# Optimization experiments

Measured on AMD Instinct MI355X. Metric: run time of the kernel, lower is better.

The kernel has to match this reference:

```python
import jax, jax.numpy as jnp
import numpy as np

N, B, S, A = 4, 32768, 512, 64
H = 256          # hidden_size
NH = 16          # effective number of heads = attend_dim (range(attend_dim) bug in source)
D = 16           # attend_dim = hidden // attend_heads
EPS_BN = 1e-5


def setup_inputs() -> dict:
    key = jax.random.key(0)
    ks = jax.random.split(key, 16)
    sc = 0.05
    return {
        "states": jax.random.normal(ks[0], (N, B, S), dtype=jnp.float32),
        "actions": jax.random.normal(ks[1], (N, B, A), dtype=jnp.float32),
        # per-agent state+action encoder (enc_fc1)
        "Wenc": jax.random.normal(ks[2], (N, S + A, H), dtype=jnp.float32) * sc,
        "benc": jax.random.normal(ks[3], (N, H), dtype=jnp.float32) * sc,
        # per-agent state encoder (s_enc_fc1)
        "Ws": jax.random.normal(ks[4], (N, S, H), dtype=jnp.float32) * sc,
        "bs": jax.random.normal(ks[5], (N, H), dtype=jnp.float32) * sc,
        # shared per-head extractors (no bias on key/selector; bias on value)
        "Wk": jax.random.normal(ks[6], (NH, H, D), dtype=jnp.float32) * sc,
        "Wsel": jax.random.normal(ks[7], (NH, H, D), dtype=jnp.float32) * sc,
        "Wv": jax.random.normal(ks[8], (NH, H, D), dtype=jnp.float32) * sc,
        "bv": jax.random.normal(ks[9], (NH, D), dtype=jnp.float32) * sc,
        # per-agent critic MLP (input = H + NH*D = 2H)
        "Wc1": jax.random.normal(ks[10], (N, 2 * H, H), dtype=jnp.float32) * sc,
        "bc1": jax.random.normal(ks[11], (N, H), dtype=jnp.float32) * sc,
        "Wc2": jax.random.normal(ks[12], (N, H, A), dtype=jnp.float32) * sc,
        "bc2": jax.random.normal(ks[13], (N, A), dtype=jnp.float32) * sc,
    }


def _lrelu(x):
    return jax.nn.leaky_relu(x, 0.01)


def _bn(x):
    # BatchNorm1d(affine=False), training mode: biased batch stats over batch axis
    m = x.mean(axis=1, keepdims=True)
    v = x.var(axis=1, keepdims=True)
    return (x - m) * jax.lax.rsqrt(v + EPS_BN)


def reference(states, actions, Wenc, benc, Ws, bs, Wk, Wsel, Wv, bv, Wc1, bc1, Wc2, bc2):
    n, b = states.shape[0], states.shape[1]
    # state+action encodings per agent: [n, B, H]
    sa = jnp.concatenate([states, actions], axis=-1)
    sa_enc = _lrelu(jnp.einsum('nbi,nih->nbh', _bn(sa), Wenc) + benc[:, None, :])
    # state encodings per agent: [n, B, H]
    s_enc = _lrelu(jnp.einsum('nbs,nsh->nbh', _bn(states), Ws) + bs[:, None, :])
    # per-head keys/values/selectors: [NH, n, B, D]
    keys = jnp.einsum('nbh,ehd->enbd', sa_enc, Wk)
    vals = _lrelu(jnp.einsum('nbh,ehd->enbd', sa_enc, Wv) + bv[:, None, None, :])
    sel = jnp.einsum('nbh,ehd->enbd', s_enc, Wsel)
    # attention of agent i over agents j != i (self excluded via -inf mask)
    logits = jnp.einsum('eibd,ejbd->eibj', sel, keys) / jnp.sqrt(jnp.float32(D))
    self_mask = jnp.eye(n, dtype=bool)[None, :, None, :]  # [1, i, 1, j]
    probs = jax.nn.softmax(jnp.where(self_mask, -1e9, logits), axis=-1)
    # weighted values: [n, B, NH, D] (head-major concat order)
    other = jnp.einsum('eibj,ejbd->ibed', probs, vals)
    critic_in = jnp.concatenate([s_enc, other.reshape(n, b, NH * D)], axis=-1)  # [n, B, 2H]
    h = _lrelu(jnp.einsum('nbc,nch->nbh', critic_in, Wc1) + bc1[:, None, :])
    all_q = jnp.einsum('nbh,nha->nba', h, Wc2) + bc2[:, None, :]  # [n, B, A]
    idx = jnp.argmax(actions, axis=-1)  # [n, B]
    q = jnp.take_along_axis(all_q, idx[..., None], axis=-1)  # [n, B, 1]
    return q
```

## Files before the change

kernel.cpp:

```cpp
#include <hip/hip_runtime.h>
#include <hip/hip_bf16.h>
#include <cstdint>
#include <cstddef>

using bf16 = __hip_bfloat16;
typedef __attribute__((ext_vector_type(8))) short bf16x8v;
typedef __attribute__((ext_vector_type(4))) short bf16x4v;
typedef __attribute__((ext_vector_type(4))) float f32x4v;

constexpr int Nn = 4;
constexpr int Bb = 32768;
constexpr int Ss = 512;
constexpr int Av = 64;
constexpr int SA = 576;
constexpr float BN_EPS = 1e-5f;

__device__ __forceinline__ float lrelu(float v){ return v >= 0.f ? v : 0.01f * v; }
__device__ __forceinline__ float bf2f(bf16 x){ return __bfloat162float(x); }
__device__ __forceinline__ short f2bf(float v){
  union { bf16 b; short s; } u; u.b = __float2bfloat16(v); return u.s;
}

template<bool WRX>
__global__ __launch_bounds__(256) void conv_stats(const float* __restrict__ states,
                                                  const float* __restrict__ actions,
                                                  float* __restrict__ ssum,
                                                  float* __restrict__ ssq,
                                                  short* __restrict__ Xbf){
  const int n  = blockIdx.z;
  const int tx = threadIdx.x;
  const int ty = threadIdx.y;
  const int g  = blockIdx.x * 64 + tx;
  const bool on = g < (SA / 4);
  const int f  = g * 4;
  const float* p = nullptr; int step = 0;
  if (on){
    if (f < Ss){ p = states  + (size_t)n*Bb*Ss + f;        step = Ss; }
    else       { p = actions + (size_t)n*Bb*Av + (f - Ss); step = Av; }
  }
  float s0=0.f,s1=0.f,s2=0.f,s3=0.f,q0=0.f,q1=0.f,q2=0.f,q3=0.f;
  const int b0 = blockIdx.y * 512 + ty, bend = blockIdx.y * 512 + 512;
  if (on){
    for (int b = b0; b < bend; b += 4){
      float4 v = *(const float4*)(p + (size_t)b*step);
      if (WRX){
        short t4[4] __attribute__((aligned(8))) =
            { f2bf(v.x), f2bf(v.y), f2bf(v.z), f2bf(v.w) };
        *(bf16x4v*)&Xbf[((size_t)n*Bb + b)*SA + f] = *(bf16x4v*)t4;
      }
      s0 += v.x; q0 += v.x*v.x;
      s1 += v.y; q1 += v.y*v.y;
      s2 += v.z; q2 += v.z*v.z;
      s3 += v.w; q3 += v.w*v.w;
    }
  }
  __shared__ float rs[4][64][4], rq[4][64][4];
  rs[ty][tx][0]=s0; rs[ty][tx][1]=s1; rs[ty][tx][2]=s2; rs[ty][tx][3]=s3;
  rq[ty][tx][0]=q0; rq[ty][tx][1]=q1; rq[ty][tx][2]=q2; rq[ty][tx][3]=q3;
  __syncthreads();
  if (ty == 0 && on){
    #pragma unroll
    for (int j = 0; j < 4; j++){
      float ts = rs[0][tx][j]+rs[1][tx][j]+rs[2][tx][j]+rs[3][tx][j];
      float tq = rq[0][tx][j]+rq[1][tx][j]+rq[2][tx][j]+rq[3][tx][j];
      atomicAdd(&ssum[n*SA + f + j], ts);
      atomicAdd(&ssq [n*SA + f + j], tq);
    }
  }
}

__global__ void bn_finalize(const float* __restrict__ ssum, const float* __restrict__ ssq,
                            float* __restrict__ mean, float* __restrict__ rstd){
  int i = blockIdx.x * 256 + threadIdx.x;
  float m = ssum[i] * (1.f / Bb);
  float v = ssq[i] * (1.f / Bb) - m * m;
  v = fmaxf(v, 0.f);
  mean[i] = m;
  rstd[i] = rsqrtf(v + BN_EPS);
}

__global__ void bias_copy(const float* __restrict__ b1, const float* __restrict__ b2,
                          float* __restrict__ o1, float* __restrict__ o2){
  int i = blockIdx.x * 256 + threadIdx.x;
  if (i < Nn*256){ o1[i] = b1[i]; o2[i] = b2[i]; }
}

template<int HEAD>
__global__ __launch_bounds__(256) void foldT2(const float* __restrict__ src,
                                              const float* __restrict__ scale,
                                              const float* __restrict__ mean,
                                              float* __restrict__ bias_out,
                                              short* __restrict__ dst,
                                              int K, int N){
  const int a  = blockIdx.z;
  const int tx = threadIdx.x & 63;
  const int ty = threadIdx.x >> 6;
  const int f0 = blockIdx.x * 64 + ty * 16;
  const int c  = blockIdx.y * 64 + tx;
  const float* s = src + (HEAD ? 0 : (size_t)a*K*N);
  short tmp[16] __attribute__((aligned(16)));
  float bsum = 0.f;
  #pragma unroll
  for (int j = 0; j < 16; j++){
    const int f = f0 + j;
    float w = HEAD ? s[(((size_t)(c >> 4))*K + f)*16 + (c & 15)]
                   : s[(size_t)f*N + c];
    if (scale) w *= scale[a*SA + f];
    if (mean)  bsum += mean[a*SA + f] * w;
    tmp[j] = f2bf(w);
  }
  short* d = dst + (HEAD ? 0 : (size_t)a*K*N) + (size_t)c*K + f0;
  *(bf16x8v*)d       = *(bf16x8v*)tmp;
  *(bf16x8v*)(d + 8) = *(bf16x8v*)(tmp + 8);
  if (mean){
    __shared__ float red[4][64];
    red[ty][tx] = bsum;
    __syncthreads();
    if (threadIdx.x < 64){
      float t = red[0][threadIdx.x] + red[1][threadIdx.x]
              + red[2][threadIdx.x] + red[3][threadIdx.x];
      atomicAdd(&bias_out[a*N + blockIdx.y*64 + threadIdx.x], -t);
    }
  }
}

template<int BM,int BN,int WM,int WN,int K,int ASRC,int AP,bool ACT,bool OUTF32>
__global__ __launch_bounds__(256) void mgemm(const void* A1, const void* A2,
                                             const short* __restrict__ Wp, int wPerAgent,
                                             const float* __restrict__ bias, int biasStride,
                                             void* Out, int outPitch){
  __shared__ __align__(16) short As[BM*40];
  __shared__ __align__(16) short Bs[BN*40];
  const int tid  = threadIdx.x;
  const int a    = blockIdx.z;
  const int row0 = blockIdx.x * BM;
  const int col0 = blockIdx.y * BN;
  const short* Wb = Wp + (size_t)a * wPerAgent;
  constexpr int FM = BM/WM/16, FN = BN/WN/16;
  const int wid = tid >> 6, lane = tid & 63;
  const int wm = wid % WM, wn = wid / WM;
  const int rowB = wm*(BM/WM), colB = wn*(BN/WN);
  const int lrow = lane & 15, lq = lane >> 4;

  f32x4v acc[FM][FN];
  #pragma unroll
  for (int i = 0; i < FM; i++)
    #pragma unroll
    for (int j = 0; j < FN; j++) acc[i][j] = (f32x4v){0.f,0.f,0.f,0.f};

  for (int k0 = 0; k0 < K; k0 += 32){
    {
      constexpr int EA = BM/8;
      int r, kq;
      if constexpr (BM == 128){ r = tid >> 1; kq = (tid & 1)*16; }
      else                    { r = tid >> 2; kq = (tid & 3)*8;  }
      const size_t grow = (size_t)a*Bb + row0 + r;
      #pragma unroll
      for (int c8 = 0; c8 < EA; c8 += 8){
        const int f = k0 + kq + c8;
        if constexpr (ASRC == 0 || ASRC == 1){
          const float* sp;
          if constexpr (ASRC == 0)
            sp = (f < 512) ? (const float*)A1 + grow*512 + f
                           : (const float*)A2 + grow*64 + (f - 512);
          else
            sp = (const float*)A1 + grow*512 + f;
          float4 x0 = *(const float4*)sp;
          float4 x1 = *(const float4*)(sp + 4);
          short tmp[8] = { f2bf(x0.x), f2bf(x0.y), f2bf(x0.z), f2bf(x0.w),
                           f2bf(x1.x), f2bf(x1.y), f2bf(x1.z), f2bf(x1.w) };
          *(bf16x8v*)&As[r*40 + kq + c8] = *(bf16x8v*)tmp;
        } else {
          const short* sp;
          if constexpr (ASRC == 3)
            sp = (f < 256) ? (const short*)A1 + grow*256 + f
                           : (const short*)A2 + grow*256 + (f - 256);
          else
            sp = (const short*)A1 + grow*(size_t)AP + f;
          *(bf16x8v*)&As[r*40 + kq + c8] = *(const bf16x8v*)sp;
        }
      }
    }
    {
      int n, kq, reps;
      if constexpr      (BN == 256){ n = tid;      kq = 0;            reps = 4; }
      else if constexpr (BN == 128){ n = tid >> 1; kq = (tid & 1)*16; reps = 2; }
      else                         { n = tid >> 2; kq = (tid & 3)*8;  reps = 1; }
      const short* wp = Wb + (size_t)(col0 + n)*K + k0 + kq;
      #pragma unroll
      for (int t = 0; t < reps; t++)
        *(bf16x8v*)&Bs[n*40 + kq + t*8] = *(const bf16x8v*)(wp + t*8);
    }
    __syncthreads();
    bf16x8v af[FM], bfr[FN];
    #pragma unroll
    for (int mi = 0; mi < FM; mi++)
      af[mi] = *(const bf16x8v*)&As[(rowB + mi*16 + lrow)*40 + lq*8];
    #pragma unroll
    for (int ni = 0; ni < FN; ni++)
      bfr[ni] = *(const bf16x8v*)&Bs[(colB + ni*16 + lrow)*40 + lq*8];
    #pragma unroll
    for (int mi = 0; mi < FM; mi++)
      #pragma unroll
      for (int ni = 0; ni < FN; ni++)
        acc[mi][ni] = __builtin_amdgcn_mfma_f32_16x16x32_bf16(af[mi], bfr[ni], acc[mi][ni], 0, 0, 0);
    __syncthreads();
  }
  #pragma unroll
  for (int mi = 0; mi < FM; mi++){
    const size_t gr = (size_t)a*Bb + row0 + rowB + mi*16 + lq*4;
    #pragma unroll
    for (int ni = 0; ni < FN; ni++){
      const int gc = col0 + colB + ni*16 + lrow;
      const float bb = bias ? bias[a*biasStride + gc] : 0.f;
      #pragma unroll
      for (int r = 0; r < 4; r++){
        float v = acc[mi][ni][r] + bb;
        if (ACT) v = lrelu(v);
        if constexpr (OUTF32) ((float*)Out)[(gr + r)*(size_t)outPitch + gc] = v;
        else                  ((bf16*) Out)[(gr + r)*(size_t)outPitch + gc] = __float2bfloat16(v);
      }
    }
  }
}

union B8g { uint4 u; bf16 h[8]; };
__global__ __launch_bounds__(256) void attn_g(const bf16* __restrict__ K_,
                                              const bf16* __restrict__ V_,
                                              bf16* SO){
  const int t = blockIdx.x * 256 + threadIdx.x;
  const int e = t & 15;
  const size_t b = t >> 4;
  const size_t ofs = b*256 + e*16;
  float S[4][16], Kf[4][16], Vf[4][16];
  #pragma unroll
  for (int i = 0; i < 4; i++){
    B8g u0, u1;
    const bf16* sp = SO + (size_t)i*Bb*256 + ofs;
    u0.u = *(const uint4*)sp; u1.u = *(const uint4*)(sp + 8);
    #pragma unroll
    for (int l = 0; l < 8; l++){ S[i][l] = bf2f(u0.h[l]); S[i][8+l] = bf2f(u1.h[l]); }
    const bf16* kp = K_ + (size_t)i*Bb*256 + ofs;
    u0.u = *(const uint4*)kp; u1.u = *(const uint4*)(kp + 8);
    #pragma unroll
    for (int l = 0; l < 8; l++){ Kf[i][l] = bf2f(u0.h[l]); Kf[i][8+l] = bf2f(u1.h[l]); }
    const bf16* vp = V_ + (size_t)i*Bb*256 + ofs;
    u0.u = *(const uint4*)vp; u1.u = *(const uint4*)(vp + 8);
    #pragma unroll
    for (int l = 0; l < 8; l++){ Vf[i][l] = bf2f(u0.h[l]); Vf[i][8+l] = bf2f(u1.h[l]); }
  }
  #pragma unroll
  for (int i = 0; i < 4; i++){
    float lg[4];
    #pragma unroll
    for (int j = 0; j < 4; j++){
      float d = 0.f;
      #pragma unroll
      for (int l = 0; l < 16; l++) d += S[i][l] * Kf[j][l];
      lg[j] = d * 0.25f;
    }
    lg[i] = -1e9f;
    float m = fmaxf(fmaxf(lg[0], lg[1]), fmaxf(lg[2], lg[3]));
    float p[4], s = 0.f;
    #pragma unroll
    for (int j = 0; j < 4; j++){ p[j] = expf(lg[j] - m); s += p[j]; }
    p[i] = 0.f;
    const float inv = 1.f / s;
    float o[16] = {};
    #pragma unroll
    for (int j = 0; j < 4; j++){
      const float pj = p[j] * inv;
      #pragma unroll
      for (int l = 0; l < 16; l++) o[l] += pj * Vf[j][l];
    }
    B8g w0, w1;
    #pragma unroll
    for (int l = 0; l < 8; l++){ w0.h[l] = __float2bfloat16(o[l]); w1.h[l] = __float2bfloat16(o[8+l]); }
    bf16* op = SO + (size_t)i*Bb*256 + ofs;
    *(uint4*)op       = w0.u;
    *(uint4*)(op + 8) = w1.u;
  }
}

__global__ __launch_bounds__(256) void sel_q(const float* __restrict__ actions,
                                             const float* __restrict__ allq,
                                             float* __restrict__ out){
  const size_t i = (size_t)blockIdx.x * 256 + threadIdx.x;
  const float* ap = actions + i*64;
  float best = ap[0]; int bi = 0;
  for (int j = 1; j < 64; j++){
    float v = ap[j];
    if (v > best){ best = v; bi = j; }
  }
  out[i] = allq[i*64 + bi];
}

constexpr int RB = 4;

template<int K>
__device__ __forceinline__ void gemm4_glb(const float* __restrict__ st,
                                          const float* __restrict__ ac,
                                          const float* __restrict__ mean,
                                          const float* __restrict__ rstd,
                                          int a, int brow0, int tid,
                                          const float* __restrict__ W,
                                          const float* __restrict__ bias, bool act,
                                          float (*Xs)[68], float (*Wt)[264],
                                          float (*Sout)[256]){
  const int r = tid >> 6, c4 = (tid & 63) * 4;
  float acc[4] = {};
  for (int k0 = 0; k0 < K; k0 += 8){
    if (tid < 32){
      const int rb = tid >> 3, kq = tid & 7;
      const int f = k0 + kq;
      float v = (f < Ss) ? st[((size_t)a*Bb + brow0 + rb)*Ss + f]
                         : ac[((size_t)a*Bb + brow0 + rb)*Av + (f - Ss)];
      Xs[kq][rb] = (v - mean[a*SA + f]) * rstd[a*SA + f];
    }
    {
      const int wk = tid >> 5, wc = (tid & 31) * 8;
      const float* wp = W + (size_t)(k0 + wk) * 256 + wc;
      *(float4*)&Wt[wk][wc]     = *(const float4*)wp;
      *(float4*)&Wt[wk][wc + 4] = *(const float4*)(wp + 4);
    }
    __syncthreads();
    #pragma unroll
    for (int kk = 0; kk < 8; kk++){
      const float av = Xs[kk][r];
      float4 w = *(const float4*)&Wt[kk][c4];
      acc[0] += av*w.x; acc[1] += av*w.y; acc[2] += av*w.z; acc[3] += av*w.w;
    }
    __syncthreads();
  }
  float4 o;
  o.x = acc[0] + (bias ? bias[c4+0] : 0.f);
  o.y = acc[1] + (bias ? bias[c4+1] : 0.f);
  o.z = acc[2] + (bias ? bias[c4+2] : 0.f);
  o.w = acc[3] + (bias ? bias[c4+3] : 0.f);
  if (act){ o.x = lrelu(o.x); o.y = lrelu(o.y); o.z = lrelu(o.z); o.w = lrelu(o.w); }
  *(float4*)&Sout[a*RB + r][c4] = o;
}

template<int K, bool HEAD>
__device__ __forceinline__ void gemm4_lds(const float (*S1)[256], const float (*S2)[256],
                                          int a, int tid,
                                          const float* __restrict__ W,
                                          const float* __restrict__ bias, bool act,
                                          float (*Wt)[264], float (*Sout)[256]){
  const int r = tid >> 6, c4 = (tid & 63) * 4;
  float acc[4] = {};
  for (int k0 = 0; k0 < K; k0 += 8){
    if (HEAD){
      const int wk = tid >> 5, c8 = (tid & 31) * 8;
      const int e = c8 >> 4, d0 = c8 & 15;
      const float* wp = W + (size_t)e*(256*16) + (size_t)(k0 + wk)*16 + d0;
      *(float4*)&Wt[wk][c8]     = *(const float4*)wp;
      *(float4*)&Wt[wk][c8 + 4] = *(const float4*)(wp + 4);
    } else {
      const int wk = tid >> 5, wc = (tid & 31) * 8;
      const float* wp = W + (size_t)(k0 + wk)*256 + wc;
      *(float4*)&Wt[wk][wc]     = *(const float4*)wp;
      *(float4*)&Wt[wk][wc + 4] = *(const float4*)(wp + 4);
    }
    __syncthreads();
    const float (*src)[256] = (k0 < 256) ? S1 : S2;
    const int kb = (k0 < 256) ? k0 : k0 - 256;
    const float* arow = &src[a*RB + r][kb];
    #pragma unroll
    for (int kk = 0; kk < 8; kk++){
      const float av = arow[kk];
      float4 w = *(const float4*)&Wt[kk][c4];
      acc[0] += av*w.x; acc[1] += av*w.y; acc[2] += av*w.z; acc[3] += av*w.w;
    }
    __syncthreads();
  }
  float4 o;
  o.x = acc[0] + (bias ? bias[c4+0] : 0.f);
  o.y = acc[1] + (bias ? bias[c4+1] : 0.f);
  o.z = acc[2] + (bias ? bias[c4+2] : 0.f);
  o.w = acc[3] + (bias ? bias[c4+3] : 0.f);
  if (act){ o.x = lrelu(o.x); o.y = lrelu(o.y); o.z = lrelu(o.z); o.w = lrelu(o.w); }
  *(float4*)&Sout[a*RB + r][c4] = o;
}

__global__ __launch_bounds__(256) void fused(
    const float* __restrict__ states, const float* __restrict__ actions,
    const float* __restrict__ mean,  const float* __restrict__ rstd,
    const float* __restrict__ Wenc, const float* __restrict__ benc,
    const float* __restrict__ Wsx,  const float* __restrict__ bsx,
    const float* __restrict__ Wk,   const float* __restrict__ Wsel,
    const float* __restrict__ Wv,   const float* __restrict__ bv,
    const float* __restrict__ Wc1,  const float* __restrict__ bc1,
    const float* __restrict__ Wc2,  const float* __restrict__ bc2,
    float* __restrict__ qout){
  __shared__ float A [16][256];
  __shared__ float Bs2[16][256];
  __shared__ float C [16][256];
  __shared__ float Wt[8][264];
  __shared__ float Xs[8][68];
  __shared__ float Cq[4][68];
  const int tid   = threadIdx.x;
  const int brow0 = blockIdx.x * RB;
  for (int a = 0; a < Nn; a++)
    gemm4_glb<Ss>(states, actions, mean, rstd, a, brow0, tid,
                  Wsx + (size_t)a*Ss*256, bsx + a*256, true, Xs, Wt, A);
  __syncthreads();
  for (int a = 0; a < Nn; a++)
    gemm4_lds<256, true>(A, nullptr, a, tid, Wsel, nullptr, false, Wt, C);
  __syncthreads();
  for (int a = 0; a < Nn; a++)
    gemm4_glb<SA>(states, actions, mean, rstd, a, brow0, tid,
                  Wenc + (size_t)a*SA*256, benc + a*256, true, Xs, Wt, A);
  __syncthreads();
  for (int a = 0; a < Nn; a++)
    gemm4_lds<256, true>(A, nullptr, a, tid, Wk, nullptr, false, Wt, Bs2);
  __syncthreads();
  for (int a = 0; a < Nn; a++)
    gemm4_lds<256, true>(A, nullptr, a, tid, Wv, bv, true, Wt, A);
  __syncthreads();
  if (tid < 64){
    const int rb = tid >> 4, e = tid & 15;
    const int co = e * 16;
    float S[4][16], Kf[4][16], Vf[4][16];
    #pragma unroll
    for (int i = 0; i < 4; i++)
      #pragma unroll
      for (int l = 0; l < 16; l++){
        S[i][l]  = C  [i*RB + rb][co + l];
        Kf[i][l] = Bs2[i*RB + rb][co + l];
        Vf[i][l] = A  [i*RB + rb][co + l];
      }
    #pragma unroll
    for (int i = 0; i < 4; i++){
      float lg[4];
      #pragma unroll
      for (int j = 0; j < 4; j++){
        float d = 0.f;
        #pragma unroll
        for (int l = 0; l < 16; l++) d += S[i][l] * Kf[j][l];
        lg[j] = d * 0.25f;
      }
      lg[i] = -1e9f;
      float m = fmaxf(fmaxf(lg[0], lg[1]), fmaxf(lg[2], lg[3]));
      float p[4], s = 0.f;
      #pragma unroll
      for (int j = 0; j < 4; j++){ p[j] = expf(lg[j] - m); s += p[j]; }
      p[i] = 0.f;
      const float inv = 1.f / s;
      float o[16] = {};
      #pragma unroll
      for (int j = 0; j < 4; j++){
        const float pj = p[j] * inv;
        #pragma unroll
        for (int l = 0; l < 16; l++) o[l] += pj * Vf[j][l];
      }
      #pragma unroll
      for (int l = 0; l < 16; l++) C[i*RB + rb][co + l] = o[l];
    }
  }
  __syncthreads();
  for (int a = 0; a < Nn; a++)
    gemm4_glb<Ss>(states, actions, mean, rstd, a, brow0, tid,
                  Wsx + (size_t)a*Ss*256, bsx + a*256, true, Xs, Wt, A);
  __syncthreads();
  for (int a = 0; a < Nn; a++)
    gemm4_lds<512, false>(A, C, a, tid, Wc1 + (size_t)a*512*256, bc1 + a*256, true, Wt, Bs2);
  __syncthreads();
  for (int a = 0; a < Nn; a++){
    const int r2 = tid >> 6, c2 = tid & 63;
    float acc = 0.f;
    for (int k0 = 0; k0 < 256; k0 += 8){
      const int wk = tid >> 5, wc = (tid & 31) * 2;
      const float* wp = Wc2 + (size_t)a*256*64 + (size_t)(k0 + wk)*64 + wc;
      Wt[wk][wc]     = wp[0];
      Wt[wk][wc + 1] = wp[1];
      __syncthreads();
      #pragma unroll
      for (int kk = 0; kk < 8; kk++) acc += Bs2[a*RB + r2][k0 + kk] * Wt[kk][c2];
      __syncthreads();
    }
    Cq[r2][c2] = acc + bc2[a*64 + c2];
    __syncthreads();
    if (tid < RB){
      const float* ap = actions + ((size_t)a*Bb + brow0 + tid)*Av;
      float best = ap[0]; int bi = 0;
      for (int j = 1; j < Av; j++){
        float v = ap[j];
        if (v > best){ best = v; bi = j; }
      }
      qout[(size_t)a*Bb + brow0 + tid] = Cq[tid][bi];
    }
    __syncthreads();
  }
}

extern "C" void kernel_launch(void* const* d_in, const int* in_sizes, int n_in,
                              void* d_out, int out_size, void* d_ws, size_t ws_size,
                              hipStream_t stream){
  (void)in_sizes; (void)n_in; (void)out_size;
  const float* states  = (const float*)d_in[0];
  const float* actions = (const float*)d_in[1];
  const float* Wenc    = (const float*)d_in[2];
  const float* benc    = (const float*)d_in[3];
  const float* Wsx     = (const float*)d_in[4];
  const float* bsx     = (const float*)d_in[5];
  const float* Wk      = (const float*)d_in[6];
  const float* Wsel    = (const float*)d_in[7];
  const float* Wv      = (const float*)d_in[8];
  const float* bv      = (const float*)d_in[9];
  const float* Wc1     = (const float*)d_in[10];
  const float* bc1     = (const float*)d_in[11];
  const float* Wc2     = (const float*)d_in[12];
  const float* bc2     = (const float*)d_in[13];
  float* qout = (float*)d_out;

  char* base = (char*)d_ws;
  float* ssum = (float*)base;
  float* ssq  = ssum + Nn*SA;
  float* mean = ssq  + Nn*SA;
  float* rstd = mean + Nn*SA;
  size_t off = 4*Nn*SA*sizeof(float);
  float* benc_p = (float*)(base + off); off += 4096;
  float* bs_p   = (float*)(base + off); off += 4096;
  short* Wenc_p = (short*)(base + off); off += (size_t)Nn*SA*256*2;
  short* Ws_p   = (short*)(base + off); off += (size_t)Nn*Ss*256*2;
  short* Whk_p  = (short*)(base + off); off += 256*256*2;
  short* Whs_p  = (short*)(base + off); off += 256*256*2;
  short* Whv_p  = (short*)(base + off); off += 256*256*2;
  short* Wc1_p  = (short*)(base + off); off += (size_t)Nn*512*256*2;
  short* Wc2_p  = (short*)(base + off); off += (size_t)Nn*64*256*2;
  const size_t BUFB = (size_t)Nn*Bb*256*2;
  const size_t XBFB = (size_t)Nn*Bb*SA*2;
  short* Xbf = (short*)(base + off);
  bf16* SEL  = (bf16*)(base + off);
  bf16* KB   = (bf16*)(base + off + BUFB);
  off += XBFB;
  bf16* S    = (bf16*)(base + off); off += BUFB;
  bf16* E    = (bf16*)(base + off); off += BUFB;
  const size_t need = off;
  float* ALLQ = (float*)E;

  hipMemsetAsync(ssum, 0, 2*Nn*SA*sizeof(float), stream);

  if (ws_size >= need){
    conv_stats<true><<<dim3(3, 64, Nn), dim3(64, 4), 0, stream>>>(states, actions, ssum, ssq, Xbf);
    bn_finalize<<<dim3(9), dim3(256), 0, stream>>>(ssum, ssq, mean, rstd);

    bias_copy<<<dim3(4), 256, 0, stream>>>(benc, bsx, benc_p, bs_p);
    foldT2<0><<<dim3(SA/64, 4, Nn), 256, 0, stream>>>(Wenc, rstd, mean, benc_p, Wenc_p, SA, 256);
    foldT2<0><<<dim3(Ss/64, 4, Nn), 256, 0, stream>>>(Wsx,  rstd, mean, bs_p,   Ws_p,  Ss, 256);
    foldT2<1><<<dim3(4, 4, 1), 256, 0, stream>>>(Wk,   nullptr, nullptr, nullptr, Whk_p, 256, 256);
    foldT2<1><<<dim3(4, 4, 1), 256, 0, stream>>>(Wsel, nullptr, nullptr, nullptr, Whs_p, 256, 256);
    foldT2<1><<<dim3(4, 4, 1), 256, 0, stream>>>(Wv,   nullptr, nullptr, nullptr, Whv_p, 256, 256);
    foldT2<0><<<dim3(8, 4, Nn), 256, 0, stream>>>(Wc1, nullptr, nullptr, nullptr, Wc1_p, 512, 256);
    foldT2<0><<<dim3(4, 1, Nn), 256, 0, stream>>>(Wc2, nullptr, nullptr, nullptr, Wc2_p, 256, 64);

    mgemm<64,256,1,4,576,2,SA,true,false><<<dim3(Bb/64, 1, Nn), 256, 0, stream>>>(
        Xbf, nullptr, Wenc_p, SA*256, benc_p, 256, E, 256);
    mgemm<64,256,1,4,512,2,SA,true,false><<<dim3(Bb/64, 1, Nn), 256, 0, stream>>>(
        Xbf, nullptr, Ws_p, Ss*256, bs_p, 256, S, 256);
    mgemm<64,256,1,4,256,2,256,false,false><<<dim3(Bb/64, 1, Nn), 256, 0, stream>>>(
        S, nullptr, Whs_p, 0, nullptr, 0, SEL, 256);
    mgemm<64,256,1,4,256,2,256,false,false><<<dim3(Bb/64, 1, Nn), 256, 0, stream>>>(
        E, nullptr, Whk_p, 0, nullptr, 0, KB, 256);
    mgemm<64,256,1,4,256,2,256,true,false><<<dim3(Bb/64, 1, Nn), 256, 0, stream>>>(
        E, nullptr, Whv_p, 0, bv, 0, E, 256);
    attn_g<<<dim3(Bb*16/256), 256, 0, stream>>>(KB, E, SEL);
    mgemm<64,256,1,4,512,3,256,true,false><<<dim3(Bb/64, 1, Nn), 256, 0, stream>>>(
        S, SEL, Wc1_p, 512*256, bc1, 256, KB, 256);
    mgemm<128,64,2,2,256,2,256,false,true><<<dim3(Bb/128, 1, Nn), 256, 0, stream>>>(
        KB, nullptr, Wc2_p, 64*256, bc2, 64, ALLQ, 64);
    sel_q<<<dim3(Nn*Bb/256), 256, 0, stream>>>(actions, ALLQ, qout);
  } else {
    conv_stats<false><<<dim3(3, 64, Nn), dim3(64, 4), 0, stream>>>(states, actions, ssum, ssq, nullptr);
    bn_finalize<<<dim3(9), dim3(256), 0, stream>>>(ssum, ssq, mean, rstd);
    fused<<<dim3(Bb/RB), 256, 0, stream>>>(states, actions, mean, rstd,
                                           Wenc, benc, Wsx, bsx,
                                           Wk, Wsel, Wv, bv,
                                           Wc1, bc1, Wc2, bc2, qout);
  }
}
```

Measured before the change: 1.046 ms.

## Merge encoder GEMMs and key/value GEMMs into wider N=512 GEMMs

The state+action and state encoders are concatenated into one N=512 weight matrix. The states-only weights are zero-padded to K=576, so one GEMM reads the bf16 input tile once and produces both encodings. The key and value head projections are likewise fused into one N=512 GEMM, with a mode flag that applies bias and leaky ReLU only to the value half. Attention and downstream GEMMs now read from the interleaved 512-wide buffers. This cuts repeated reads of the activations and kernel launches, at the cost of larger LDS tiles, more accumulator registers per block, and some wasted MFMA work on the zero-padded K rows.

```diff
diff --git a/kernel.cpp b/kernel.cpp
--- a/kernel.cpp
+++ b/kernel.cpp
@@ -79,10 +79,13 @@
   rstd[i] = rsqrtf(v + BN_EPS);
 }
 
-__global__ void bias_copy(const float* __restrict__ b1, const float* __restrict__ b2,
-                          float* __restrict__ o1, float* __restrict__ o2){
+__global__ void bias_copy(const float* __restrict__ benc, const float* __restrict__ bsx,
+                          float* __restrict__ besc){
   int i = blockIdx.x * 256 + threadIdx.x;
-  if (i < Nn*256){ o1[i] = b1[i]; o2[i] = b2[i]; }
+  if (i < Nn*512){
+    int a = i >> 9, c = i & 511;
+    besc[i] = (c < 256) ? benc[a*256 + c] : bsx[a*256 + (c - 256)];
+  }
 }
 
 template<int HEAD>
@@ -91,25 +94,29 @@
                                               const float* __restrict__ mean,
                                               float* __restrict__ bias_out,
                                               short* __restrict__ dst,
-                                              int K, int N){
+                                              int Ks, int Kd, int N,
+                                              int aDst, int biasStride){
   const int a  = blockIdx.z;
   const int tx = threadIdx.x & 63;
   const int ty = threadIdx.x >> 6;
   const int f0 = blockIdx.x * 64 + ty * 16;
   const int c  = blockIdx.y * 64 + tx;
-  const float* s = src + (HEAD ? 0 : (size_t)a*K*N);
+  const float* s = src + (HEAD ? 0 : (size_t)a*Ks*N);
   short tmp[16] __attribute__((aligned(16)));
   float bsum = 0.f;
   #pragma unroll
   for (int j = 0; j < 16; j++){
     const int f = f0 + j;
-    float w = HEAD ? s[(((size_t)(c >> 4))*K + f)*16 + (c & 15)]
-                   : s[(size_t)f*N + c];
-    if (scale) w *= scale[a*SA + f];
-    if (mean)  bsum += mean[a*SA + f] * w;
+    float w = 0.f;
+    if (f < Ks){
+      w = HEAD ? s[(((size_t)(c >> 4))*Ks + f)*16 + (c & 15)]
+               : s[(size_t)f*N + c];
+      if (scale) w *= scale[a*SA + f];
+      if (mean)  bsum += mean[a*SA + f] * w;
+    }
     tmp[j] = f2bf(w);
   }
-  short* d = dst + (HEAD ? 0 : (size_t)a*K*N) + (size_t)c*K + f0;
+  short* d = dst + (size_t)a*aDst + (size_t)c*Kd + f0;
   *(bf16x8v*)d       = *(bf16x8v*)tmp;
   *(bf16x8v*)(d + 8) = *(bf16x8v*)(tmp + 8);
   if (mean){
@@ -119,12 +126,12 @@
     if (threadIdx.x < 64){
       float t = red[0][threadIdx.x] + red[1][threadIdx.x]
               + red[2][threadIdx.x] + red[3][threadIdx.x];
-      atomicAdd(&bias_out[a*N + blockIdx.y*64 + threadIdx.x], -t);
-    }
-  }
-}
-
-template<int BM,int BN,int WM,int WN,int K,int ASRC,int AP,bool ACT,bool OUTF32>
+      atomicAdd(&bias_out[a*biasStride + blockIdx.y*64 + threadIdx.x], -t);
+    }
+  }
+}
+
+template<int BM,int BN,int WM,int WN,int K,int ASRC,int AP,bool ACT,bool OUTF32,int MODE>
 __global__ __launch_bounds__(256) void mgemm(const void* A1, const void* A2,
                                              const short* __restrict__ Wp, int wPerAgent,
                                              const float* __restrict__ bias, int biasStride,
@@ -158,38 +165,35 @@
       #pragma unroll
       for (int c8 = 0; c8 < EA; c8 += 8){
         const int f = k0 + kq + c8;
-        if constexpr (ASRC == 0 || ASRC == 1){
-          const float* sp;
-          if constexpr (ASRC == 0)
-            sp = (f < 512) ? (const float*)A1 + grow*512 + f
-                           : (const float*)A2 + grow*64 + (f - 512);
-          else
-            sp = (const float*)A1 + grow*512 + f;
-          float4 x0 = *(const float4*)sp;
-          float4 x1 = *(const float4*)(sp + 4);
-          short tmp[8] = { f2bf(x0.x), f2bf(x0.y), f2bf(x0.z), f2bf(x0.w),
-                           f2bf(x1.x), f2bf(x1.y), f2bf(x1.z), f2bf(x1.w) };
-          *(bf16x8v*)&As[r*40 + kq + c8] = *(bf16x8v*)tmp;
-        } else {
-          const short* sp;
-          if constexpr (ASRC == 3)
-            sp = (f < 256) ? (const short*)A1 + grow*256 + f
-                           : (const short*)A2 + grow*256 + (f - 256);
-          else
-            sp = (const short*)A1 + grow*(size_t)AP + f;
-          *(bf16x8v*)&As[r*40 + kq + c8] = *(const bf16x8v*)sp;
+        const short* sp;
+        if constexpr (ASRC == 3)
+          sp = (f < 256) ? (const short*)A1 + grow*(size_t)AP + f
+                         : (const short*)A2 + grow*256 + (f - 256);
+        else
+          sp = (const short*)A1 + grow*(size_t)AP + f;
+        *(bf16x8v*)&As[r*40 + kq + c8] = *(const bf16x8v*)sp;
+      }
+    }
+    {
+      if constexpr (BN == 512){
+        const int n = tid;
+        #pragma unroll
+        for (int h = 0; h < 2; h++){
+          const short* wp = Wb + (size_t)(col0 + n + h*256)*K + k0;
+          #pragma unroll
+          for (int t = 0; t < 4; t++)
+            *(bf16x8v*)&Bs[(n + h*256)*40 + t*8] = *(const bf16x8v*)(wp + t*8);
         }
-      }
-    }
-    {
-      int n, kq, reps;
-      if constexpr      (BN == 256){ n = tid;      kq = 0;            reps = 4; }
-      else if constexpr (BN == 128){ n = tid >> 1; kq = (tid & 1)*16; reps = 2; }
-      else                         { n = tid >> 2; kq = (tid & 3)*8;  reps = 1; }
-      const short* wp = Wb + (size_t)(col0 + n)*K + k0 + kq;
-      #pragma unroll
-      for (int t = 0; t < reps; t++)
-        *(bf16x8v*)&Bs[n*40 + kq + t*8] = *(const bf16x8v*)(wp + t*8);
+      } else {
+        int n, kq, reps;
+        if constexpr      (BN == 256){ n = tid;      kq = 0;            reps = 4; }
+        else if constexpr (BN == 128){ n = tid >> 1; kq = (tid & 1)*16; reps = 2; }
+        else                         { n = tid >> 2; kq = (tid & 3)*8;  reps = 1; }
+        const short* wp = Wb + (size_t)(col0 + n)*K + k0 + kq;
+        #pragma unroll
+        for (int t = 0; t < reps; t++)
+          *(bf16x8v*)&Bs[n*40 + kq + t*8] = *(const bf16x8v*)(wp + t*8);
+      }
     }
     __syncthreads();
     bf16x8v af[FM], bfr[FN];
@@ -212,11 +216,18 @@
     #pragma unroll
     for (int ni = 0; ni < FN; ni++){
       const int gc = col0 + colB + ni*16 + lrow;
-      const float bb = bias ? bias[a*biasStride + gc] : 0.f;
+      float bb; bool doact;
+      if constexpr (MODE == 1){
+        doact = (gc >= 256);
+        bb = doact ? bias[gc - 256] : 0.f;
+      } else {
+        bb = bias ? bias[a*biasStride + gc] : 0.f;
+        doact = ACT;
+      }
       #pragma unroll
       for (int r = 0; r < 4; r++){
         float v = acc[mi][ni][r] + bb;
-        if (ACT) v = lrelu(v);
+        if (doact) v = lrelu(v);
         if constexpr (OUTF32) ((float*)Out)[(gr + r)*(size_t)outPitch + gc] = v;
         else                  ((bf16*) Out)[(gr + r)*(size_t)outPitch + gc] = __float2bfloat16(v);
       }
@@ -225,26 +236,26 @@
 }
 
 union B8g { uint4 u; bf16 h[8]; };
-__global__ __launch_bounds__(256) void attn_g(const bf16* __restrict__ K_,
-                                              const bf16* __restrict__ V_,
+__global__ __launch_bounds__(256) void attn_g(const bf16* __restrict__ KV,
                                               bf16* SO){
   const int t = blockIdx.x * 256 + threadIdx.x;
   const int e = t & 15;
   const size_t b = t >> 4;
-  const size_t ofs = b*256 + e*16;
+  const size_t ofsKV = b*512 + e*16;
+  const size_t ofsS  = b*256 + e*16;
   float S[4][16], Kf[4][16], Vf[4][16];
   #pragma unroll
   for (int i = 0; i < 4; i++){
     B8g u0, u1;
-    const bf16* sp = SO + (size_t)i*Bb*256 + ofs;
+    const bf16* sp = SO + (size_t)i*Bb*256 + ofsS;
     u0.u = *(const uint4*)sp; u1.u = *(const uint4*)(sp + 8);
     #pragma unroll
     for (int l = 0; l < 8; l++){ S[i][l] = bf2f(u0.h[l]); S[i][8+l] = bf2f(u1.h[l]); }
-    const bf16* kp = K_ + (size_t)i*Bb*256 + ofs;
+    const bf16* kp = KV + (size_t)i*Bb*512 + ofsKV;
     u0.u = *(const uint4*)kp; u1.u = *(const uint4*)(kp + 8);
     #pragma unroll
     for (int l = 0; l < 8; l++){ Kf[i][l] = bf2f(u0.h[l]); Kf[i][8+l] = bf2f(u1.h[l]); }
-    const bf16* vp = V_ + (size_t)i*Bb*256 + ofs;
+    const bf16* vp = kp + 256;
     u0.u = *(const uint4*)vp; u1.u = *(const uint4*)(vp + 8);
     #pragma unroll
     for (int l = 0; l < 8; l++){ Vf[i][l] = bf2f(u0.h[l]); Vf[i][8+l] = bf2f(u1.h[l]); }
@@ -276,7 +287,7 @@
     B8g w0, w1;
     #pragma unroll
     for (int l = 0; l < 8; l++){ w0.h[l] = __float2bfloat16(o[l]); w1.h[l] = __float2bfloat16(o[8+l]); }
-    bf16* op = SO + (size_t)i*Bb*256 + ofs;
+    bf16* op = SO + (size_t)i*Bb*256 + ofsS;
     *(uint4*)op       = w0.u;
     *(uint4*)(op + 8) = w1.u;
   }
@@ -520,25 +531,22 @@
   float* mean = ssq  + Nn*SA;
   float* rstd = mean + Nn*SA;
   size_t off = 4*Nn*SA*sizeof(float);
-  float* benc_p = (float*)(base + off); off += 4096;
-  float* bs_p   = (float*)(base + off); off += 4096;
-  short* Wenc_p = (short*)(base + off); off += (size_t)Nn*SA*256*2;
-  short* Ws_p   = (short*)(base + off); off += (size_t)Nn*Ss*256*2;
-  short* Whk_p  = (short*)(base + off); off += 256*256*2;
-  short* Whs_p  = (short*)(base + off); off += 256*256*2;
-  short* Whv_p  = (short*)(base + off); off += 256*256*2;
-  short* Wc1_p  = (short*)(base + off); off += (size_t)Nn*512*256*2;
-  short* Wc2_p  = (short*)(base + off); off += (size_t)Nn*64*256*2;
-  const size_t BUFB = (size_t)Nn*Bb*256*2;
+  float* besc  = (float*)(base + off); off += Nn*512*sizeof(float);
+  short* Wes_p = (short*)(base + off); off += (size_t)Nn*512*SA*2;
+  short* Wkv_p = (short*)(base + off); off += 512*256*2;
+  short* Whs_p = (short*)(base + off); off += 256*256*2;
+  short* Wc1_p = (short*)(base + off); off += (size_t)Nn*256*512*2;
+  short* Wc2_p = (short*)(base + off); off += (size_t)Nn*64*256*2;
   const size_t XBFB = (size_t)Nn*Bb*SA*2;
+  const size_t W512 = (size_t)Nn*Bb*512*2;
   short* Xbf = (short*)(base + off);
-  bf16* SEL  = (bf16*)(base + off);
-  bf16* KB   = (bf16*)(base + off + BUFB);
+  bf16*  SEL = (bf16*)(base + off);
+  float* ALLQ= (float*)(base + off);
   off += XBFB;
-  bf16* S    = (bf16*)(base + off); off += BUFB;
-  bf16* E    = (bf16*)(base + off); off += BUFB;
+  bf16* ES = (bf16*)(base + off); off += W512;
+  bf16* KV = (bf16*)(base + off); off += W512;
+  bf16* H  = KV;
   const size_t need = off;
-  float* ALLQ = (float*)E;
 
   hipMemsetAsync(ssum, 0, 2*Nn*SA*sizeof(float), stream);
 
@@ -546,30 +554,26 @@
     conv_stats<true><<<dim3(3, 64, Nn), dim3(64, 4), 0, stream>>>(states, actions, ssum, ssq, Xbf);
     bn_finalize<<<dim3(9), dim3(256), 0, stream>>>(ssum, ssq, mean, rstd);
 
-    bias_copy<<<dim3(4), 256, 0, stream>>>(benc, bsx, benc_p, bs_p);
-    foldT2<0><<<dim3(SA/64, 4, Nn), 256, 0, stream>>>(Wenc, rstd, mean, benc_p, Wenc_p, SA, 256);
-    foldT2<0><<<dim3(Ss/64, 4, Nn), 256, 0, stream>>>(Wsx,  rstd, mean, bs_p,   Ws_p,  Ss, 256);
-    foldT2<1><<<dim3(4, 4, 1), 256, 0, stream>>>(Wk,   nullptr, nullptr, nullptr, Whk_p, 256, 256);
-    foldT2<1><<<dim3(4, 4, 1), 256, 0, stream>>>(Wsel, nullptr, nullptr, nullptr, Whs_p, 256, 256);
-    foldT2<1><<<dim3(4, 4, 1), 256, 0, stream>>>(Wv,   nullptr, nullptr, nullptr, Whv_p, 256, 256);
-    foldT2<0><<<dim3(8, 4, Nn), 256, 0, stream>>>(Wc1, nullptr, nullptr, nullptr, Wc1_p, 512, 256);
-    foldT2<0><<<dim3(4, 1, Nn), 256, 0, stream>>>(Wc2, nullptr, nullptr, nullptr, Wc2_p, 256, 64);
-
-    mgemm<64,256,1,4,576,2,SA,true,false><<<dim3(Bb/64, 1, Nn), 256, 0, stream>>>(
-        Xbf, nullptr, Wenc_p, SA*256, benc_p, 256, E, 256);
-    mgemm<64,256,1,4,512,2,SA,true,false><<<dim3(Bb/64, 1, Nn), 256, 0, stream>>>(
-        Xbf, nullptr, Ws_p, Ss*256, bs_p, 256, S, 256);
-    mgemm<64,256,1,4,256,2,256,false,false><<<dim3(Bb/64, 1, Nn), 256, 0, stream>>>(
-        S, nullptr, Whs_p, 0, nullptr, 0, SEL, 256);
-    mgemm<64,256,1,4,256,2,256,false,false><<<dim3(Bb/64, 1, Nn), 256, 0, stream>>>(
-        E, nullptr, Whk_p, 0, nullptr, 0, KB, 256);
-    mgemm<64,256,1,4,256,2,256,true,false><<<dim3(Bb/64, 1, Nn), 256, 0, stream>>>(
-        E, nullptr, Whv_p, 0, bv, 0, E, 256);
-    attn_g<<<dim3(Bb*16/256), 256, 0, stream>>>(KB, E, SEL);
-    mgemm<64,256,1,4,512,3,256,true,false><<<dim3(Bb/64, 1, Nn), 256, 0, stream>>>(
-        S, SEL, Wc1_p, 512*256, bc1, 256, KB, 256);
-    mgemm<128,64,2,2,256,2,256,false,true><<<dim3(Bb/128, 1, Nn), 256, 0, stream>>>(
-        KB, nullptr, Wc2_p, 64*256, bc2, 64, ALLQ, 64);
+    bias_copy<<<dim3(8), 256, 0, stream>>>(benc, bsx, besc);
+    foldT2<0><<<dim3(9, 4, Nn), 256, 0, stream>>>(Wenc, rstd, mean, besc,       Wes_p,            SA, SA, 256, 512*SA, 512);
+    foldT2<0><<<dim3(9, 4, Nn), 256, 0, stream>>>(Wsx,  rstd, mean, besc + 256, Wes_p + 256*SA,   Ss, SA, 256, 512*SA, 512);
+    foldT2<1><<<dim3(4, 4, 1), 256, 0, stream>>>(Wk,   nullptr, nullptr, nullptr, Wkv_p,           256, 256, 256, 0, 0);
+    foldT2<1><<<dim3(4, 4, 1), 256, 0, stream>>>(Wv,   nullptr, nullptr, nullptr, Wkv_p + 256*256, 256, 256, 256, 0, 0);
+    foldT2<1><<<dim3(4, 4, 1), 256, 0, stream>>>(Wsel, nullptr, nullptr, nullptr, Whs_p,           256, 256, 256, 0, 0);
+    foldT2<0><<<dim3(8, 4, Nn), 256, 0, stream>>>(Wc1, nullptr, nullptr, nullptr, Wc1_p,           512, 512, 256, 256*512, 0);
+    foldT2<0><<<dim3(4, 1, Nn), 256, 0, stream>>>(Wc2, nullptr, nullptr, nullptr, Wc2_p,           256, 256, 64,  64*256,  0);
+
+    mgemm<64,512,1,4,576,2,SA,true,false,0><<<dim3(Bb/64, 1, Nn), 256, 0, stream>>>(
+        Xbf, nullptr, Wes_p, 512*SA, besc, 512, ES, 512);
+    mgemm<64,512,1,4,256,2,512,false,false,1><<<dim3(Bb/64, 1, Nn), 256, 0, stream>>>(
+        ES, nullptr, Wkv_p, 0, bv, 0, KV, 512);
+    mgemm<64,256,1,4,256,2,512,false,false,0><<<dim3(Bb/64, 1, Nn), 256, 0, stream>>>(
+        (const short*)ES + 256, nullptr, Whs_p, 0, nullptr, 0, SEL, 256);
+    attn_g<<<dim3(Bb*16/256), 256, 0, stream>>>(KV, SEL);
+    mgemm<64,256,1,4,512,3,512,true,false,0><<<dim3(Bb/64, 1, Nn), 256, 0, stream>>>(
+        (const short*)ES + 256, SEL, Wc1_p, 256*512, bc1, 256, H, 256);
+    mgemm<128,64,2,2,256,2,256,false,true,0><<<dim3(Bb/128, 1, Nn), 256, 0, stream>>>(
+        H, nullptr, Wc2_p, 64*256, bc2, 64, ALLQ, 64);
     sel_q<<<dim3(Nn*Bb/256), 256, 0, stream>>>(actions, ALLQ, qout);
   } else {
     conv_stats<false><<<dim3(3, 64, Nn), dim3(64, 4), 0, stream>>>(states, actions, ssum, ssq, nullptr);
```

Result: slower. 1.225 ms (+17.1%).
